# Kernel tuning notes

Hardware: AMD Instinct MI355X
Metric: run time of the kernel (lower is better)

Reference implementation:

```python
import jax, jax.numpy as jnp
import numpy as np

N_NODES = 100000
N_EDGES = 600000
HIDDEN = 128
ALPHA = 0.1
K_HOPS = 10


def setup_inputs() -> dict:
    key = jax.random.key(0)
    k1, k2, k3, k4 = jax.random.split(key, 4)
    x = jax.random.normal(k1, (N_NODES, HIDDEN), dtype=jnp.float32)
    edge_index = jax.random.randint(k2, (2, N_EDGES), 0, N_NODES, dtype=jnp.int64)
    W = jax.random.normal(k3, (HIDDEN, HIDDEN), dtype=jnp.float32) * (1.0 / np.sqrt(HIDDEN))
    b = jax.random.normal(k4, (HIDDEN,), dtype=jnp.float32) * 0.01
    return {"x": x, "edge_index": edge_index, "W": W, "b": b}


def reference(x, edge_index, W, b):
    N = x.shape[0]
    # Linear projection (PyTorch convention: y = x W^T + b)
    h = x @ W.T + b

    # gcn_norm with added self-loops (PyG APPNPConv default)
    loop = jnp.arange(N, dtype=edge_index.dtype)
    src = jnp.concatenate([edge_index[0], loop])  # [E+N]
    dst = jnp.concatenate([edge_index[1], loop])
    ones = jnp.ones(src.shape[0], dtype=h.dtype)
    deg = jax.ops.segment_sum(ones, dst, num_segments=N)  # in-degree incl. self-loop
    dinv = jnp.where(deg > 0, jax.lax.rsqrt(deg), 0.0)
    norm = dinv[src] * dinv[dst]  # [E+N]

    # APPNP propagation: h <- (1-alpha) * A_hat h + alpha * h0
    h0 = h
    for _ in range(K_HOPS):
        msg = norm[:, None] * h[src]  # gather + scale
        agg = jax.ops.segment_sum(msg, dst, num_segments=N)  # scatter-add
        h = (1.0 - ALPHA) * agg + ALPHA * h0
    return h
```

## Files before the change

### kernel.cpp

```cpp
#include <hip/hip_runtime.h>

#define N_NODES_C 100000
#define N_EDGES_C 600000
#define HIDDEN_C 128
#define K_HOPS_C 10
#define SCAN_B 98

typedef short short8 __attribute__((ext_vector_type(8)));
typedef float f32x16 __attribute__((ext_vector_type(16)));

__device__ __forceinline__ unsigned short f2bf(float f) {
    unsigned u = __float_as_uint(f);
    return (unsigned short)((u + 0x7FFFu + ((u >> 16) & 1u)) >> 16);
}
__device__ __forceinline__ float bf_lo(unsigned p) { return __uint_as_float(p << 16); }
__device__ __forceinline__ float bf_hi(unsigned p) { return __uint_as_float(p & 0xFFFF0000u); }

__global__ void k_deg(const int* __restrict__ dst, int* __restrict__ deg, int E) {
    int e = blockIdx.x * blockDim.x + threadIdx.x;
    if (e < E) atomicAdd(&deg[dst[e]], 1);
}

__global__ __launch_bounds__(1024) void k_scan_a(const int* __restrict__ deg,
                                                 int* __restrict__ offs,
                                                 int* __restrict__ blksum,
                                                 float* __restrict__ dinv, int N) {
    __shared__ int wtot[16];
    int tid = threadIdx.x;
    int i = blockIdx.x * 1024 + tid;
    int lane = tid & 63;
    int wid = tid >> 6;
    int v = (i < N) ? deg[i] : 0;
    if (i < N) dinv[i] = rsqrtf((float)(v + 1));
    int incl = v;
#pragma unroll
    for (int d = 1; d < 64; d <<= 1) {
        int t = __shfl_up(incl, (unsigned)d, 64);
        if (lane >= d) incl += t;
    }
    if (lane == 63) wtot[wid] = incl;
    __syncthreads();
    int woff = 0, btot = 0;
#pragma unroll
    for (int w = 0; w < 16; ++w) {
        int t = wtot[w];
        if (w < wid) woff += t;
        btot += t;
    }
    if (i < N) offs[i] = woff + incl - v;
    if (tid == 0) blksum[blockIdx.x] = btot;
}

__global__ __launch_bounds__(128) void k_scan_b(const int* __restrict__ blksum,
                                                int* __restrict__ blkoff,
                                                int* __restrict__ offs, int NB, int N) {
    __shared__ int wt[2];
    int t = threadIdx.x;
    int lane = t & 63;
    int w = t >> 6;
    int v = (t < NB) ? blksum[t] : 0;
    int incl = v;
#pragma unroll
    for (int d = 1; d < 64; d <<= 1) {
        int s = __shfl_up(incl, (unsigned)d, 64);
        if (lane >= d) incl += s;
    }
    if (lane == 63) wt[w] = incl;
    __syncthreads();
    int excl = incl - v + (w == 1 ? wt[0] : 0);
    if (t < NB) blkoff[t] = excl;
    if (t == 127) offs[N] = wt[0] + wt[1];
}

__global__ __launch_bounds__(1024) void k_scan_c(int* __restrict__ offs,
                                                 int* __restrict__ cursor,
                                                 const int* __restrict__ blkoff, int N) {
    int i = blockIdx.x * 1024 + threadIdx.x;
    if (i < N) {
        int v = offs[i] + blkoff[blockIdx.x];
        offs[i] = v;
        cursor[i] = v;
    }
}

__global__ void k_fill(const int* __restrict__ src, const int* __restrict__ dst,
                       const float* __restrict__ dinv, int* __restrict__ cursor,
                       uint2* __restrict__ csr, int E) {
    int e = blockIdx.x * blockDim.x + threadIdx.x;
    if (e < E) {
        int s = src[e], d = dst[e];
        int pos = atomicAdd(&cursor[d], 1);
        uint2 v;
        v.x = (unsigned)s;
        v.y = __float_as_uint(dinv[s] * dinv[d]);
        csr[pos] = v;
    }
}

__global__ __launch_bounds__(256) void k_gemm(const float* __restrict__ x,
                                              const float* __restrict__ W,
                                              const float* __restrict__ b,
                                              unsigned short* __restrict__ hb, int N) {
    __shared__ unsigned short Wb[HIDDEN_C * HIDDEN_C];
    int tid = threadIdx.x;
#pragma unroll
    for (int i = 0; i < 8; ++i) {
        int c = tid + 256 * i;
        int m = c >> 4;
        int g = c & 15;
        const float4* wsrc = (const float4*)W + m * 32 + g * 2;
        float4 wa = wsrc[0];
        float4 wb = wsrc[1];
        unsigned short t8[8];
        t8[0] = f2bf(wa.x); t8[1] = f2bf(wa.y); t8[2] = f2bf(wa.z); t8[3] = f2bf(wa.w);
        t8[4] = f2bf(wb.x); t8[5] = f2bf(wb.y); t8[6] = f2bf(wb.z); t8[7] = f2bf(wb.w);
        int gs = g ^ (m & 15);
        *(uint4*)&Wb[m * 128 + gs * 8] = *(const uint4*)t8;
    }
    __syncthreads();

    int lane = tid & 63;
    int wv = tid >> 6;
    int row0 = blockIdx.x * 128 + wv * 32;
    int m = lane & 31;
    int half = lane >> 5;

    int row = row0 + m;
    if (row >= N) row = N - 1;
    const float4* xrow = (const float4*)(x + (size_t)row * 128);

    f32x16 acc[4];
#pragma unroll
    for (int t = 0; t < 4; ++t)
#pragma unroll
        for (int r = 0; r < 16; ++r) acc[t][r] = 0.f;

    for (int s = 0; s < 8; ++s) {
        int kb = s * 16 + half * 8;
        float4 x0 = xrow[kb >> 2];
        float4 x1 = xrow[(kb >> 2) + 1];
        union { unsigned short u[8]; short8 v; } af;
        af.u[0] = f2bf(x0.x); af.u[1] = f2bf(x0.y); af.u[2] = f2bf(x0.z); af.u[3] = f2bf(x0.w);
        af.u[4] = f2bf(x1.x); af.u[5] = f2bf(x1.y); af.u[6] = f2bf(x1.z); af.u[7] = f2bf(x1.w);
        int g = kb >> 3;
#pragma unroll
        for (int t = 0; t < 4; ++t) {
            int r = t * 32 + m;
            short8 bfrag = *(const short8*)&Wb[r * 128 + ((g ^ (r & 15)) << 3)];
            acc[t] = __builtin_amdgcn_mfma_f32_32x32x16_bf16(af.v, bfrag, acc[t], 0, 0, 0);
        }
    }

    float bias[4];
#pragma unroll
    for (int t = 0; t < 4; ++t) bias[t] = b[t * 32 + m];
#pragma unroll
    for (int t = 0; t < 4; ++t) {
#pragma unroll
        for (int r = 0; r < 16; ++r) {
            int rrow = (r & 3) + 8 * (r >> 2) + 4 * half;
            int node = row0 + rrow;
            if (node < N) {
                float v = acc[t][r] + bias[t];
                hb[(size_t)node * 128 + t * 32 + m] = f2bf(v);
            }
        }
    }
}

__global__ __launch_bounds__(256) void k_prop(const uint4* __restrict__ hin4,
                                              const uint4* __restrict__ h04,
                                              uint4* __restrict__ hout_b,
                                              float* __restrict__ hout_f,
                                              const int* __restrict__ offs,
                                              const uint2* __restrict__ csr,
                                              const float* __restrict__ dinv,
                                              int N, int final_hop) {
    int tid = threadIdx.x;
    int lane = tid & 63;
    int wid = tid >> 6;
    int node = blockIdx.x * 4 + wid;
    if (node >= N) return;

    int q = lane >> 4;
    int f = lane & 15;

    int beg = offs[node];
    int end = offs[node + 1];

    uint4 hq = make_uint4(0u, 0u, 0u, 0u);
    uint4 ps = make_uint4(0u, 0u, 0u, 0u);
    float ws = 0.f;
    if (q == 0) {
        hq = h04[(size_t)node * 16 + f];
        ps = hin4[(size_t)node * 16 + f];
        float dv = dinv[node];
        ws = dv * dv;
    }

    float acc[8];
#pragma unroll
    for (int i = 0; i < 8; ++i) acc[i] = 0.f;

    int j = beg;
    for (; j + 8 <= end; j += 8) {
        uint2 e0 = csr[j + q];
        uint2 e1 = csr[j + q + 4];
        uint4 p0 = hin4[(size_t)e0.x * 16 + f];
        uint4 p1 = hin4[(size_t)e1.x * 16 + f];
        float w0 = __uint_as_float(e0.y);
        float w1 = __uint_as_float(e1.y);
        acc[0] += w0 * bf_lo(p0.x); acc[1] += w0 * bf_hi(p0.x);
        acc[2] += w0 * bf_lo(p0.y); acc[3] += w0 * bf_hi(p0.y);
        acc[4] += w0 * bf_lo(p0.z); acc[5] += w0 * bf_hi(p0.z);
        acc[6] += w0 * bf_lo(p0.w); acc[7] += w0 * bf_hi(p0.w);
        acc[0] += w1 * bf_lo(p1.x); acc[1] += w1 * bf_hi(p1.x);
        acc[2] += w1 * bf_lo(p1.y); acc[3] += w1 * bf_hi(p1.y);
        acc[4] += w1 * bf_lo(p1.z); acc[5] += w1 * bf_hi(p1.z);
        acc[6] += w1 * bf_lo(p1.w); acc[7] += w1 * bf_hi(p1.w);
    }
    if (j < end) {
        int jj0 = j + q;
        int jj1 = j + q + 4;
        if (jj0 < end) {
            uint2 e = csr[jj0];
            uint4 p = hin4[(size_t)e.x * 16 + f];
            float w = __uint_as_float(e.y);
            acc[0] += w * bf_lo(p.x); acc[1] += w * bf_hi(p.x);
            acc[2] += w * bf_lo(p.y); acc[3] += w * bf_hi(p.y);
            acc[4] += w * bf_lo(p.z); acc[5] += w * bf_hi(p.z);
            acc[6] += w * bf_lo(p.w); acc[7] += w * bf_hi(p.w);
        }
        if (jj1 < end) {
            uint2 e = csr[jj1];
            uint4 p = hin4[(size_t)e.x * 16 + f];
            float w = __uint_as_float(e.y);
            acc[0] += w * bf_lo(p.x); acc[1] += w * bf_hi(p.x);
            acc[2] += w * bf_lo(p.y); acc[3] += w * bf_hi(p.y);
            acc[4] += w * bf_lo(p.z); acc[5] += w * bf_hi(p.z);
            acc[6] += w * bf_lo(p.w); acc[7] += w * bf_hi(p.w);
        }
    }

    acc[0] += ws * bf_lo(ps.x); acc[1] += ws * bf_hi(ps.x);
    acc[2] += ws * bf_lo(ps.y); acc[3] += ws * bf_hi(ps.y);
    acc[4] += ws * bf_lo(ps.z); acc[5] += ws * bf_hi(ps.z);
    acc[6] += ws * bf_lo(ps.w); acc[7] += ws * bf_hi(ps.w);

#pragma unroll
    for (int i = 0; i < 8; ++i) {
        acc[i] += __shfl_xor(acc[i], 16, 64);
        acc[i] += __shfl_xor(acc[i], 32, 64);
    }

    if (q == 0) {
        float o[8];
        o[0] = 0.9f * acc[0] + 0.1f * bf_lo(hq.x);
        o[1] = 0.9f * acc[1] + 0.1f * bf_hi(hq.x);
        o[2] = 0.9f * acc[2] + 0.1f * bf_lo(hq.y);
        o[3] = 0.9f * acc[3] + 0.1f * bf_hi(hq.y);
        o[4] = 0.9f * acc[4] + 0.1f * bf_lo(hq.z);
        o[5] = 0.9f * acc[5] + 0.1f * bf_hi(hq.z);
        o[6] = 0.9f * acc[6] + 0.1f * bf_lo(hq.w);
        o[7] = 0.9f * acc[7] + 0.1f * bf_hi(hq.w);
        if (final_hop) {
            float4* dst0 = (float4*)(hout_f + (size_t)node * 128 + f * 8);
            float4 v0; v0.x = o[0]; v0.y = o[1]; v0.z = o[2]; v0.w = o[3];
            float4 v1; v1.x = o[4]; v1.y = o[5]; v1.z = o[6]; v1.w = o[7];
            dst0[0] = v0;
            dst0[1] = v1;
        } else {
            uint4 p;
            p.x = (unsigned)f2bf(o[0]) | ((unsigned)f2bf(o[1]) << 16);
            p.y = (unsigned)f2bf(o[2]) | ((unsigned)f2bf(o[3]) << 16);
            p.z = (unsigned)f2bf(o[4]) | ((unsigned)f2bf(o[5]) << 16);
            p.w = (unsigned)f2bf(o[6]) | ((unsigned)f2bf(o[7]) << 16);
            hout_b[(size_t)node * 16 + f] = p;
        }
    }
}

extern "C" void kernel_launch(void* const* d_in, const int* in_sizes, int n_in,
                              void* d_out, int out_size, void* d_ws, size_t ws_size,
                              hipStream_t stream) {
    const float* x = (const float*)d_in[0];
    const int* edge = (const int*)d_in[1];
    const float* W = (const float*)d_in[2];
    const float* b = (const float*)d_in[3];
    float* out = (float*)d_out;

    const int N = N_NODES_C;
    const int E = N_EDGES_C;
    const int* src = edge;
    const int* dst = edge + E;

    char* ws = (char*)d_ws;
    size_t off = 0;
    auto carve = [&](size_t bytes) -> void* {
        void* p = ws + off;
        off = (off + bytes + 511) & ~(size_t)511;
        return p;
    };
    unsigned short* h0b = (unsigned short*)carve((size_t)N * HIDDEN_C * 2);
    unsigned short* bA  = (unsigned short*)carve((size_t)N * HIDDEN_C * 2);
    unsigned short* bB  = (unsigned short*)carve((size_t)N * HIDDEN_C * 2);
    int*   deg     = (int*)  carve((size_t)N * sizeof(int));
    float* dinv    = (float*)carve((size_t)N * sizeof(float));
    int*   offs    = (int*)  carve((size_t)(N + 1) * sizeof(int));
    int*   cursor  = (int*)  carve((size_t)N * sizeof(int));
    uint2* csr     = (uint2*)carve((size_t)E * sizeof(uint2));
    int*   blksum  = (int*)  carve((size_t)SCAN_B * sizeof(int));
    int*   blkoff  = (int*)  carve((size_t)SCAN_B * sizeof(int));
    (void)ws_size;

    hipMemsetAsync(deg, 0, (size_t)N * sizeof(int), stream);

    int eb = (E + 255) / 256;
    k_deg<<<eb, 256, 0, stream>>>(dst, deg, E);
    k_scan_a<<<SCAN_B, 1024, 0, stream>>>(deg, offs, blksum, dinv, N);
    k_scan_b<<<1, 128, 0, stream>>>(blksum, blkoff, offs, SCAN_B, N);
    k_scan_c<<<SCAN_B, 1024, 0, stream>>>(offs, cursor, blkoff, N);
    k_fill<<<eb, 256, 0, stream>>>(src, dst, dinv, cursor, csr, E);

    k_gemm<<<(N + 127) / 128, 256, 0, stream>>>(x, W, b, h0b, N);

    const uint4* hin = (const uint4*)h0b;
    for (int k = 0; k < K_HOPS_C; ++k) {
        int fin = (k == K_HOPS_C - 1);
        uint4* houtb = ((k & 1) == 0) ? (uint4*)bA : (uint4*)bB;
        k_prop<<<(N + 3) / 4, 256, 0, stream>>>(hin, (const uint4*)h0b,
                                                fin ? nullptr : houtb,
                                                fin ? out : nullptr,
                                                offs, csr, dinv, N, fin);
        hin = houtb;
    }
}
```

Baseline: 573.4 us.

## Map one node per 16-lane quarter-wave in propagation kernel

Each 16-lane group of a wavefront now handles its own destination node instead of a whole wave splitting one node's edges across four quarters. This drops the cross-lane shuffle reduction and the idle lanes at the writeback, and launches a quarter as many blocks. In exchange, the four nodes in a wave have different degrees, so lanes diverge on loop trip count, and each quarter walks its edge list serially with less memory-level parallelism per node.

```diff
diff --git a/kernel.cpp b/kernel.cpp
--- a/kernel.cpp
+++ b/kernel.cpp
@@ -179,19 +179,22 @@
     int tid = threadIdx.x;
     int lane = tid & 63;
     int wid = tid >> 6;
-    int node = blockIdx.x * 4 + wid;
-    if (node >= N) return;
-
     int q = lane >> 4;
     int f = lane & 15;
 
-    int beg = offs[node];
-    int end = offs[node + 1];
+    int node = (blockIdx.x * 4 + wid) * 4 + q;
+    bool valid = node < N;
+
+    int beg = 0, end = 0;
+    if (valid) {
+        beg = offs[node];
+        end = offs[node + 1];
+    }
 
     uint4 hq = make_uint4(0u, 0u, 0u, 0u);
     uint4 ps = make_uint4(0u, 0u, 0u, 0u);
     float ws = 0.f;
-    if (q == 0) {
+    if (valid) {
         hq = h04[(size_t)node * 16 + f];
         ps = hin4[(size_t)node * 16 + f];
         float dv = dinv[node];
@@ -203,9 +206,10 @@
     for (int i = 0; i < 8; ++i) acc[i] = 0.f;
 
     int j = beg;
-    for (; j + 8 <= end; j += 8) {
-        uint2 e0 = csr[j + q];
-        uint2 e1 = csr[j + q + 4];
+#pragma unroll 2
+    for (; j + 2 <= end; j += 2) {
+        uint2 e0 = csr[j];
+        uint2 e1 = csr[j + 1];
         uint4 p0 = hin4[(size_t)e0.x * 16 + f];
         uint4 p1 = hin4[(size_t)e1.x * 16 + f];
         float w0 = __uint_as_float(e0.y);
@@ -220,26 +224,13 @@
         acc[6] += w1 * bf_lo(p1.w); acc[7] += w1 * bf_hi(p1.w);
     }
     if (j < end) {
-        int jj0 = j + q;
-        int jj1 = j + q + 4;
-        if (jj0 < end) {
-            uint2 e = csr[jj0];
-            uint4 p = hin4[(size_t)e.x * 16 + f];
-            float w = __uint_as_float(e.y);
-            acc[0] += w * bf_lo(p.x); acc[1] += w * bf_hi(p.x);
-            acc[2] += w * bf_lo(p.y); acc[3] += w * bf_hi(p.y);
-            acc[4] += w * bf_lo(p.z); acc[5] += w * bf_hi(p.z);
-            acc[6] += w * bf_lo(p.w); acc[7] += w * bf_hi(p.w);
-        }
-        if (jj1 < end) {
-            uint2 e = csr[jj1];
-            uint4 p = hin4[(size_t)e.x * 16 + f];
-            float w = __uint_as_float(e.y);
-            acc[0] += w * bf_lo(p.x); acc[1] += w * bf_hi(p.x);
-            acc[2] += w * bf_lo(p.y); acc[3] += w * bf_hi(p.y);
-            acc[4] += w * bf_lo(p.z); acc[5] += w * bf_hi(p.z);
-            acc[6] += w * bf_lo(p.w); acc[7] += w * bf_hi(p.w);
-        }
+        uint2 e = csr[j];
+        uint4 p = hin4[(size_t)e.x * 16 + f];
+        float w = __uint_as_float(e.y);
+        acc[0] += w * bf_lo(p.x); acc[1] += w * bf_hi(p.x);
+        acc[2] += w * bf_lo(p.y); acc[3] += w * bf_hi(p.y);
+        acc[4] += w * bf_lo(p.z); acc[5] += w * bf_hi(p.z);
+        acc[6] += w * bf_lo(p.w); acc[7] += w * bf_hi(p.w);
     }
 
     acc[0] += ws * bf_lo(ps.x); acc[1] += ws * bf_hi(ps.x);
@@ -247,13 +238,7 @@
     acc[4] += ws * bf_lo(ps.z); acc[5] += ws * bf_hi(ps.z);
     acc[6] += ws * bf_lo(ps.w); acc[7] += ws * bf_hi(ps.w);
 
-#pragma unroll
-    for (int i = 0; i < 8; ++i) {
-        acc[i] += __shfl_xor(acc[i], 16, 64);
-        acc[i] += __shfl_xor(acc[i], 32, 64);
-    }
-
-    if (q == 0) {
+    if (valid) {
         float o[8];
         o[0] = 0.9f * acc[0] + 0.1f * bf_lo(hq.x);
         o[1] = 0.9f * acc[1] + 0.1f * bf_hi(hq.x);
@@ -328,10 +313,10 @@
     for (int k = 0; k < K_HOPS_C; ++k) {
         int fin = (k == K_HOPS_C - 1);
         uint4* houtb = ((k & 1) == 0) ? (uint4*)bA : (uint4*)bB;
-        k_prop<<<(N + 3) / 4, 256, 0, stream>>>(hin, (const uint4*)h0b,
-                                                fin ? nullptr : houtb,
-                                                fin ? out : nullptr,
-                                                offs, csr, dinv, N, fin);
+        k_prop<<<(N + 15) / 16, 256, 0, stream>>>(hin, (const uint4*)h0b,
+                                                  fin ? nullptr : houtb,
+                                                  fin ? out : nullptr,
+                                                  offs, csr, dinv, N, fin);
         hin = houtb;
     }
 }
```

After: 509.8 us. -11.1%, faster.
